# Optimization experiments

Hardware: AMD Instinct MI355X
Metric: run time of the kernel (lower is better)

## Reference

```python
import jax, jax.numpy as jnp
import numpy as np

KERNEL = 8


def setup_inputs() -> dict:
    key = jax.random.key(0)
    ks = jax.random.split(key, 9)
    N, Cin, L = 16, 128, 2048
    Cout = 256
    x = jax.random.normal(ks[0], (N, Cin, L), dtype=jnp.float32)
    conv_w = jax.random.normal(ks[1], (Cout, Cin, KERNEL), dtype=jnp.float32) * (1.0 / np.sqrt(Cin * KERNEL))
    conv_b = jax.random.normal(ks[2], (Cout,), dtype=jnp.float32) * 0.01
    wq = jax.random.normal(ks[3], (Cout, Cout), dtype=jnp.float32) * (1.0 / np.sqrt(Cout))
    bq = jax.random.normal(ks[4], (Cout,), dtype=jnp.float32) * 0.01
    wk = jax.random.normal(ks[5], (Cout, Cout), dtype=jnp.float32) * (1.0 / np.sqrt(Cout))
    bk = jax.random.normal(ks[6], (Cout,), dtype=jnp.float32) * 0.01
    wv = jax.random.normal(ks[7], (Cout, Cout), dtype=jnp.float32) * (1.0 / np.sqrt(Cout))
    bv = jax.random.normal(ks[8], (Cout,), dtype=jnp.float32) * 0.01
    return {"x": x, "conv_w": conv_w, "conv_b": conv_b,
            "wq": wq, "bq": bq, "wk": wk, "bk": bk, "wv": wv, "bv": bv}


def reference(x, conv_w, conv_b, wq, bq, wk, bk, wv, bv):
    # Conv1d, valid padding: [N, Cin, L] -> [N, Cout, S], S = L - KERNEL + 1
    h = jax.lax.conv_general_dilated(
        x, conv_w, window_strides=(1,), padding='VALID',
        dimension_numbers=('NCH', 'OIH', 'NCH'))
    h = jax.nn.relu(h + conv_b[None, :, None])
    N, C, S = h.shape
    h = jnp.transpose(h, (0, 2, 1))  # [N, S, C]
    # Linear layers (torch convention: y = x @ W^T + b)
    q = jnp.einsum('nsc,dc->nsd', h, wq) + bq
    k = jnp.einsum('nsc,dc->nsd', h, wk) + bk
    v = jnp.einsum('nsc,dc->nsd', h, wv) + bv
    # sigmoid (non-normalized) attention over full SxS scores
    scores = jnp.einsum('nsd,ntd->nst', q, k) / jnp.sqrt(jnp.asarray(C, h.dtype))
    attn = jax.nn.sigmoid(scores)  # [N, S, S]
    out = jnp.einsum('nst,ntd->nsd', attn, v)
    return jnp.transpose(out, (0, 2, 1))  # [N, C, S]
```

## Files before the change

### kernel.cpp

```cpp
#include <hip/hip_runtime.h>

typedef short short8 __attribute__((ext_vector_type(8)));
typedef float f32x4 __attribute__((ext_vector_type(4)));
typedef float f32x16 __attribute__((ext_vector_type(16)));
typedef unsigned short u16x4 __attribute__((ext_vector_type(4)));

constexpr int NB = 16, CIN = 128, LIN = 2048, CO = 256;
constexpr int SL = 2041;
constexpr int MT = NB * SL;
constexpr int MP = 32768;
constexpr int XTS = 136;

constexpr size_t XT_OFF = 0;
constexpr size_t XT_SZ  = (size_t)NB*LIN*XTS*2 + 65536;
constexpr size_t CW_OFF = XT_OFF + XT_SZ;
constexpr size_t CW_SZ  = (size_t)CO*CIN*8*2;
constexpr size_t WQ_OFF = CW_OFF + CW_SZ;
constexpr size_t WB_SZ  = (size_t)CO*CO*2;
constexpr size_t WK_OFF = WQ_OFF + WB_SZ;
constexpr size_t WV_OFF = WK_OFF + WB_SZ;
constexpr size_t H_OFF  = WV_OFF + WB_SZ;
constexpr size_t HB_SZ  = (size_t)MP*CO*2;
constexpr size_t Q_OFF  = H_OFF + HB_SZ;
constexpr size_t K_OFF  = Q_OFF + HB_SZ;
constexpr size_t VT_OFF = K_OFF + HB_SZ;

__device__ inline unsigned short f2bf(float f) {
  union { float f; unsigned int u; } v; v.f = f;
  unsigned int r = v.u + 0x7fffu + ((v.u >> 16) & 1u);
  return (unsigned short)(r >> 16);
}

__device__ inline void sync_lds() {
  __asm__ volatile("" ::: "memory");
  __builtin_amdgcn_s_waitcnt(0xc07f);
  __builtin_amdgcn_s_barrier();
  __asm__ volatile("" ::: "memory");
}
__device__ inline void barrier_only() {
  __asm__ volatile("" ::: "memory");
  __builtin_amdgcn_s_barrier();
  __asm__ volatile("" ::: "memory");
}

#if defined(__has_builtin)
#if __has_builtin(__builtin_amdgcn_global_load_lds)
#define HAVE_GLDS 1
#endif
#endif

__device__ inline void gld16(const unsigned short* g, void* l) {
#ifdef HAVE_GLDS
  __builtin_amdgcn_global_load_lds(
      (const __attribute__((address_space(1))) void*)g,
      (__attribute__((address_space(3))) void*)l, 16, 0, 0);
#else
  *(short8*)l = *(const short8*)g;
#endif
}

__global__ void xpose_kernel(const float* __restrict__ x, unsigned short* __restrict__ xt) {
  __shared__ float tile[32][33];
  const int tx = threadIdx.x, ty = threadIdx.y;
  const int s0 = blockIdx.x * 32, c0 = blockIdx.y * 32, n = blockIdx.z;
  #pragma unroll
  for (int r = 0; r < 4; ++r)
    tile[ty * 4 + r][tx] = x[((size_t)(n * CIN + c0 + ty * 4 + r)) * LIN + s0 + tx];
  __syncthreads();
  #pragma unroll
  for (int r = 0; r < 4; ++r)
    xt[((size_t)(n * LIN + s0 + ty * 4 + r)) * XTS + c0 + tx] = f2bf(tile[tx][ty * 4 + r]);
}

__global__ void wconv_kernel(const float* __restrict__ w, unsigned short* __restrict__ o) {
  int idx = blockIdx.x * 256 + threadIdx.x;
  int co = idx >> 10, r = idx & 1023, kp = r >> 7, ci = r & 127;
  o[idx] = f2bf(w[co * 1024 + ci * 8 + kp]);
}

__global__ void wqkv_kernel(const float* __restrict__ a, const float* __restrict__ b,
                            const float* __restrict__ c, unsigned short* __restrict__ oa,
                            unsigned short* __restrict__ ob, unsigned short* __restrict__ oc) {
  int z = blockIdx.x >> 6, lb = blockIdx.x & 63;
  const float* src = (z == 0) ? a : (z == 1) ? b : c;
  unsigned short* dst = (z == 0) ? oa : (z == 1) ? ob : oc;
  int i = (lb * 256 + threadIdx.x) * 4;
  float4 v = *(const float4*)(src + i);
  u16x4 r;
  r.x = f2bf(v.x); r.y = f2bf(v.y); r.z = f2bf(v.z); r.w = f2bf(v.w);
  *(u16x4*)(dst + i) = r;
}

__global__ __launch_bounds__(256) void conv_gemm(
    const unsigned short* __restrict__ xt,
    const unsigned short* __restrict__ wb,
    const float* __restrict__ bias,
    unsigned short* __restrict__ h)
{
  __shared__ unsigned short sX[18432];
  __shared__ unsigned short sB[2][4096];
  const int tid = threadIdx.x;
  const int w = tid >> 6, lane = tid & 63, quad = lane >> 4, l16 = lane & 15;
  const int n  = blockIdx.y;
  const int s0 = blockIdx.x * 128;
  const int d0 = blockIdx.z * 128;

  {
    const unsigned short* xbase = xt + ((size_t)n * LIN + s0) * XTS;
    #pragma unroll
    for (int i = 0; i < 9; ++i) {
      int u = i * 256 + tid;
      gld16(xbase + u * 8, ((char*)sX) + u * 16);
    }
  }

  const int brow0 = tid >> 2, bkgs = tid & 3;
  short8 breg[2];
  #pragma unroll
  for (int i2 = 0; i2 < 2; ++i2) {
    int row = i2 * 64 + brow0;
    int kg = bkgs ^ ((row >> 1) & 3);
    breg[i2] = *(const short8*)(wb + (size_t)(d0 + row) * 1024 + kg * 8);
  }
  #pragma unroll
  for (int i2 = 0; i2 < 2; ++i2)
    *(short8*)(&sB[0][(i2 * 256 + tid) * 8]) = breg[i2];
  __syncthreads();

  f32x4 acc[2][8];
  #pragma unroll
  for (int i = 0; i < 2; ++i)
    #pragma unroll
    for (int j = 0; j < 8; ++j) acc[i][j] = (f32x4){0.f, 0.f, 0.f, 0.f};

  for (int kc = 0; kc < 32; ++kc) {
    const int kcn = (kc < 31) ? kc + 1 : kc;
    const int kpn = kcn >> 2, ci0n = (kcn & 3) * 32;
    #pragma unroll
    for (int i2 = 0; i2 < 2; ++i2) {
      int row = i2 * 64 + brow0;
      int kg = bkgs ^ ((row >> 1) & 3);
      breg[i2] = *(const short8*)(wb + (size_t)(d0 + row) * 1024 + kpn * 128 + ci0n + kg * 8);
    }

    const int kp = kc >> 2, ci0 = (kc & 3) * 32;
    const unsigned short* sBc = sB[kc & 1];
    short8 bfr[8];
    #pragma unroll
    for (int j = 0; j < 8; ++j) {
      int r = j * 16 + l16;
      bfr[j] = *(const short8*)(sBc + r * 32 + (quad ^ ((r >> 1) & 3)) * 8);
    }
    #pragma unroll
    for (int i = 0; i < 2; ++i) {
      int srow = w * 32 + i * 16 + l16;
      short8 afr = *(const short8*)(sX + (srow + kp) * XTS + ci0 + quad * 8);
      #pragma unroll
      for (int j = 0; j < 8; ++j)
        acc[i][j] = __builtin_amdgcn_mfma_f32_16x16x32_bf16(afr, bfr[j], acc[i][j], 0, 0, 0);
    }

    #pragma unroll
    for (int i2 = 0; i2 < 2; ++i2)
      *(short8*)(&sB[(kc + 1) & 1][(i2 * 256 + tid) * 8]) = breg[i2];
    sync_lds();
  }

  #pragma unroll
  for (int i = 0; i < 2; ++i)
    #pragma unroll
    for (int j = 0; j < 8; ++j) {
      int col = d0 + j * 16 + l16;
      float bv = bias[col];
      #pragma unroll
      for (int jj = 0; jj < 4; ++jj) {
        int s = s0 + w * 32 + i * 16 + quad * 4 + jj;
        if (s < SL) {
          float val = fmaxf(acc[i][j][jj] + bv, 0.f);
          h[(size_t)(n * SL + s) * CO + col] = f2bf(val);
        }
      }
    }
}

__global__ __launch_bounds__(256) void lin_gemm(
    const unsigned short* __restrict__ A,
    const unsigned short* __restrict__ Bq, const unsigned short* __restrict__ Bk,
    const unsigned short* __restrict__ Bv,
    const float* __restrict__ biq, const float* __restrict__ bik,
    const float* __restrict__ biv,
    unsigned short* __restrict__ qb, unsigned short* __restrict__ kb,
    unsigned short* __restrict__ vtb)
{
  __shared__ unsigned short sA[2][4096];
  __shared__ unsigned short sB[2][4096];
  const int tid = threadIdx.x;
  const int w = tid >> 6, lane = tid & 63, quad = lane >> 4, l16 = lane & 15;
  const int m0 = blockIdx.x * 128, d0 = blockIdx.y * 128, z = blockIdx.z;
  const unsigned short* B = (z == 0) ? Bq : (z == 1) ? Bk : Bv;
  const float* bias        = (z == 0) ? biq : (z == 1) ? bik : biv;

  const int brow0 = tid >> 2, bkgs = tid & 3;
  short8 areg[2], breg[2];
  #pragma unroll
  for (int i2 = 0; i2 < 2; ++i2) {
    int row = i2 * 64 + brow0;
    int kg = bkgs ^ ((row >> 1) & 3);
    areg[i2] = *(const short8*)(A + (size_t)(m0 + row) * CO + kg * 8);
    breg[i2] = *(const short8*)(B + (size_t)(d0 + row) * CO + kg * 8);
  }
  #pragma unroll
  for (int i2 = 0; i2 < 2; ++i2) {
    *(short8*)(&sA[0][(i2 * 256 + tid) * 8]) = areg[i2];
    *(short8*)(&sB[0][(i2 * 256 + tid) * 8]) = breg[i2];
  }
  sync_lds();

  f32x4 acc[2][8];
  #pragma unroll
  for (int i = 0; i < 2; ++i)
    #pragma unroll
    for (int j = 0; j < 8; ++j) acc[i][j] = (f32x4){0.f, 0.f, 0.f, 0.f};

  for (int kc = 0; kc < 8; ++kc) {
    const int kcn = (kc < 7) ? kc + 1 : kc;
    #pragma unroll
    for (int i2 = 0; i2 < 2; ++i2) {
      int row = i2 * 64 + brow0;
      int kg = bkgs ^ ((row >> 1) & 3);
      areg[i2] = *(const short8*)(A + (size_t)(m0 + row) * CO + kcn * 32 + kg * 8);
      breg[i2] = *(const short8*)(B + (size_t)(d0 + row) * CO + kcn * 32 + kg * 8);
    }

    const unsigned short* sAc = sA[kc & 1];
    const unsigned short* sBc = sB[kc & 1];
    short8 afr[2], bfr[8];
    #pragma unroll
    for (int i = 0; i < 2; ++i) {
      int r = w * 32 + i * 16 + l16;
      afr[i] = *(const short8*)(sAc + r * 32 + (quad ^ ((r >> 1) & 3)) * 8);
    }
    #pragma unroll
    for (int j = 0; j < 8; ++j) {
      int r = j * 16 + l16;
      bfr[j] = *(const short8*)(sBc + r * 32 + (quad ^ ((r >> 1) & 3)) * 8);
    }
    #pragma unroll
    for (int i = 0; i < 2; ++i)
      #pragma unroll
      for (int j = 0; j < 8; ++j)
        acc[i][j] = __builtin_amdgcn_mfma_f32_16x16x32_bf16(afr[i], bfr[j], acc[i][j], 0, 0, 0);

    #pragma unroll
    for (int i2 = 0; i2 < 2; ++i2) {
      *(short8*)(&sA[(kc + 1) & 1][(i2 * 256 + tid) * 8]) = areg[i2];
      *(short8*)(&sB[(kc + 1) & 1][(i2 * 256 + tid) * 8]) = breg[i2];
    }
    sync_lds();
  }

  #pragma unroll
  for (int i = 0; i < 2; ++i)
    #pragma unroll
    for (int j = 0; j < 8; ++j) {
      int col = d0 + j * 16 + l16;
      float bv = bias[col];
      #pragma unroll
      for (int jj = 0; jj < 4; ++jj) {
        int m = m0 + w * 32 + i * 16 + quad * 4 + jj;
        float val = acc[i][j][jj] + bv;
        if (z < 2) {
          ((z == 0) ? qb : kb)[(size_t)m * CO + col] = f2bf(val);
        } else if (m < MT) {
          int nn = m / SL, ss = m - nn * SL;
          vtb[(size_t)col * MP + nn * 2048 + ss] = f2bf(val);
        }
      }
    }
}

__global__ __launch_bounds__(512, 2) void attn_kernel(
    const unsigned short* __restrict__ qb,
    const unsigned short* __restrict__ kb,
    const unsigned short* __restrict__ vtb,
    float* __restrict__ out)
{
  __shared__ unsigned short sK[2][16384];
  __shared__ unsigned short sV[2][16384];
  __shared__ unsigned short sP[8192];
  const int tid = threadIdx.x;
  const int w = tid >> 6, lane = tid & 63;
  const int half = lane >> 5, l32 = lane & 31;
  const int bidx = blockIdx.x;
  const int n = (bidx & 7) + ((bidx >> 7) << 3);
  const int s0 = ((bidx >> 3) & 15) * 128;
  const int sr = w & 3, tr = w >> 2;

  const unsigned short* kbN = kb + (size_t)(n * SL) * CO;
  const unsigned short* vbN = vtb + (size_t)n * 2048;

#define STAGE_TILE(buf, tk)                                                      \
  {                                                                              \
    _Pragma("unroll")                                                            \
    for (int i = 0; i < 4; ++i) {                                                \
      int u = i * 512 + tid;                                                     \
      int t = u >> 5, sl = u & 31;                                               \
      gld16(kbN + (size_t)((tk) + t) * CO + ((sl ^ (t & 31)) << 3),              \
            ((char*)sK[buf]) + u * 16);                                          \
    }                                                                            \
    _Pragma("unroll")                                                            \
    for (int i = 0; i < 4; ++i) {                                                \
      int u = i * 512 + tid;                                                     \
      int d = u >> 3, sl = u & 7;                                                \
      gld16(vbN + (size_t)d * MP + (tk) + ((sl ^ (d & 7)) << 3),                 \
            ((char*)sV[buf]) + u * 16);                                          \
    }                                                                            \
  }

  STAGE_TILE(0, 0)

  short8 qf[16];
  {
    const unsigned short* qp = qb + (size_t)(n * SL + s0 + sr * 32 + l32) * CO + half * 8;
    #pragma unroll
    for (int kk = 0; kk < 16; ++kk) qf[kk] = *(const short8*)(qp + kk * 16);
  }

  __builtin_amdgcn_s_waitcnt(0x0F70);
  barrier_only();

  f32x16 o[4];
  #pragma unroll
  for (int di = 0; di < 4; ++di)
    #pragma unroll
    for (int r = 0; r < 16; ++r) o[di][r] = 0.f;

  for (int it = 0; it < 32; ++it) {
    const int cur = it & 1;
    if (it < 31) {
      STAGE_TILE(cur ^ 1, (it + 1) * 64)
      __builtin_amdgcn_s_waitcnt(0x0F78);
    } else {
      __builtin_amdgcn_s_waitcnt(0x0F70);
    }
    barrier_only();

    const unsigned short* sKc = sK[cur];
    const int tl = tr * 32 + l32;
    f32x16 sacc;
    #pragma unroll
    for (int r = 0; r < 16; ++r) sacc[r] = 0.f;
    #pragma unroll
    for (int kk = 0; kk < 16; ++kk) {
      short8 kf = *(const short8*)(sKc + tl * 256 + (((kk * 2 + half) ^ (tl & 31)) << 3));
      sacc = __builtin_amdgcn_mfma_f32_32x32x16_bf16(kf, qf[kk], sacc, 0, 0, 0);
    }

    const int t0 = it * 64;
    #pragma unroll
    for (int q2 = 0; q2 < 4; ++q2) {
      u16x4 pk;
      #pragma unroll
      for (int e = 0; e < 4; ++e) {
        int tg = t0 + tr * 32 + 8 * q2 + 4 * half + e;
        float p = __builtin_amdgcn_rcpf(1.f + __expf(-sacc[q2 * 4 + e] * 0.0625f));
        pk[e] = (tg < SL) ? f2bf(p) : (unsigned short)0;
      }
      *(u16x4*)(sP + ((tr * 4 + q2) * 128 + sr * 32 + l32) * 8 + 4 * half) = pk;
    }
    sync_lds();

    const unsigned short* sVc = sV[cur];
    #pragma unroll
    for (int kt = 0; kt < 4; ++kt) {
      int g = kt * 2 + half;
      short8 pa = *(const short8*)(sP + ((g << 7) + sr * 32 + l32) * 8);
      #pragma unroll
      for (int di = 0; di < 4; ++di) {
        int d = tr * 128 + di * 32 + l32;
        short8 vf = *(const short8*)(sVc + d * 64 + ((g ^ (d & 7)) << 3));
        o[di] = __builtin_amdgcn_mfma_f32_32x32x16_bf16(vf, pa, o[di], 0, 0, 0);
      }
    }
    sync_lds();
  }

  const int s = s0 + sr * 32 + l32;
  if (s < SL) {
    float* op = out + (size_t)n * CO * SL + s;
    #pragma unroll
    for (int di = 0; di < 4; ++di)
      #pragma unroll
      for (int r = 0; r < 16; ++r) {
        int d = tr * 128 + di * 32 + (r & 3) + 8 * (r >> 2) + 4 * half;
        __builtin_nontemporal_store(o[di][r], op + (size_t)d * SL);
      }
  }
#undef STAGE_TILE
}

extern "C" void kernel_launch(void* const* d_in, const int* in_sizes, int n_in,
                              void* d_out, int out_size, void* d_ws, size_t ws_size,
                              hipStream_t stream) {
  const float* x      = (const float*)d_in[0];
  const float* conv_w = (const float*)d_in[1];
  const float* conv_b = (const float*)d_in[2];
  const float* wq     = (const float*)d_in[3];
  const float* bq     = (const float*)d_in[4];
  const float* wk     = (const float*)d_in[5];
  const float* bk     = (const float*)d_in[6];
  const float* wv     = (const float*)d_in[7];
  const float* bv     = (const float*)d_in[8];

  char* ws = (char*)d_ws;
  unsigned short* xt  = (unsigned short*)(ws + XT_OFF);
  unsigned short* cw  = (unsigned short*)(ws + CW_OFF);
  unsigned short* wqb = (unsigned short*)(ws + WQ_OFF);
  unsigned short* wkb = (unsigned short*)(ws + WK_OFF);
  unsigned short* wvb = (unsigned short*)(ws + WV_OFF);
  unsigned short* hb  = (unsigned short*)(ws + H_OFF);
  unsigned short* qb  = (unsigned short*)(ws + Q_OFF);
  unsigned short* kb  = (unsigned short*)(ws + K_OFF);
  unsigned short* vtb = (unsigned short*)(ws + VT_OFF);

  hipLaunchKernelGGL(xpose_kernel, dim3(64, 4, 16), dim3(32, 8), 0, stream, x, xt);
  hipLaunchKernelGGL(wconv_kernel, dim3(1024), dim3(256), 0, stream, conv_w, cw);
  hipLaunchKernelGGL(wqkv_kernel,  dim3(192), dim3(256), 0, stream,
                     wq, wk, wv, wqb, wkb, wvb);
  hipLaunchKernelGGL(conv_gemm, dim3(16, 16, 2), dim3(256), 0, stream, xt, cw, conv_b, hb);
  hipLaunchKernelGGL(lin_gemm,  dim3(256, 2, 3), dim3(256), 0, stream,
                     hb, wqb, wkb, wvb, bq, bk, bv, qb, kb, vtb);
  hipLaunchKernelGGL(attn_kernel, dim3(256), dim3(512), 0, stream,
                     qb, kb, vtb, (float*)d_out);
}
```

Measured before the change: 250.8 us.

## Keep sigmoid probabilities in registers and split PV over key halves

The 1/sqrt(C) scale is folded into the Q projection epilogue. The attention loop now converts sigmoid scores to bf16 in registers with packed convert and permlane32 swaps, so the LDS round-trip through sP is gone. Each warp group now accumulates all 256 output dims over its own half of the key tile instead of half the dims over all keys. The two partial outputs are reduced through LDS at the end. The prefetch wait moves to after the PV MFMAs and s_setprio is added around the MFMA blocks. This doubles the output accumulator registers (8 f32x16) and adds a final cross-warp reduction, which may raise register pressure under launch_bounds(512,2).

```diff
diff --git a/kernel.cpp b/kernel.cpp
--- a/kernel.cpp
+++ b/kernel.cpp
@@ -57,6 +57,15 @@
 #else
   *(short8*)l = *(const short8*)g;
 #endif
+}
+
+__device__ inline unsigned int cvt_pk_bf16(float a, float b) {
+  unsigned int r;
+  asm("v_cvt_pk_bf16_f32 %0, %1, %2" : "=v"(r) : "v"(a), "v"(b));
+  return r;
+}
+__device__ inline void swap32(unsigned int& a, unsigned int& b) {
+  asm("v_permlane32_swap_b32 %0, %1" : "+v"(a), "+v"(b));
 }
 
 __global__ void xpose_kernel(const float* __restrict__ x, unsigned short* __restrict__ xt) {
@@ -269,8 +278,10 @@
       for (int jj = 0; jj < 4; ++jj) {
         int m = m0 + w * 32 + i * 16 + quad * 4 + jj;
         float val = acc[i][j][jj] + bv;
-        if (z < 2) {
-          ((z == 0) ? qb : kb)[(size_t)m * CO + col] = f2bf(val);
+        if (z == 0) {
+          qb[(size_t)m * CO + col] = f2bf(val * 0.0625f);
+        } else if (z == 1) {
+          kb[(size_t)m * CO + col] = f2bf(val);
         } else if (m < MT) {
           int nn = m / SL, ss = m - nn * SL;
           vtb[(size_t)col * MP + nn * 2048 + ss] = f2bf(val);
@@ -287,7 +298,6 @@
 {
   __shared__ unsigned short sK[2][16384];
   __shared__ unsigned short sV[2][16384];
-  __shared__ unsigned short sP[8192];
   const int tid = threadIdx.x;
   const int w = tid >> 6, lane = tid & 63;
   const int half = lane >> 5, l32 = lane & 31;
@@ -329,72 +339,109 @@
   __builtin_amdgcn_s_waitcnt(0x0F70);
   barrier_only();
 
-  f32x16 o[4];
-  #pragma unroll
-  for (int di = 0; di < 4; ++di)
+  f32x16 o[8];
+  #pragma unroll
+  for (int di = 0; di < 8; ++di)
     #pragma unroll
     for (int r = 0; r < 16; ++r) o[di][r] = 0.f;
 
   for (int it = 0; it < 32; ++it) {
     const int cur = it & 1;
-    if (it < 31) {
-      STAGE_TILE(cur ^ 1, (it + 1) * 64)
-      __builtin_amdgcn_s_waitcnt(0x0F78);
-    } else {
-      __builtin_amdgcn_s_waitcnt(0x0F70);
-    }
-    barrier_only();
+    if (it < 31) STAGE_TILE(cur ^ 1, (it + 1) * 64)
 
     const unsigned short* sKc = sK[cur];
     const int tl = tr * 32 + l32;
     f32x16 sacc;
     #pragma unroll
     for (int r = 0; r < 16; ++r) sacc[r] = 0.f;
+    __builtin_amdgcn_s_setprio(1);
     #pragma unroll
     for (int kk = 0; kk < 16; ++kk) {
       short8 kf = *(const short8*)(sKc + tl * 256 + (((kk * 2 + half) ^ (tl & 31)) << 3));
       sacc = __builtin_amdgcn_mfma_f32_32x32x16_bf16(kf, qf[kk], sacc, 0, 0, 0);
     }
-
-    const int t0 = it * 64;
-    #pragma unroll
-    for (int q2 = 0; q2 < 4; ++q2) {
-      u16x4 pk;
-      #pragma unroll
-      for (int e = 0; e < 4; ++e) {
-        int tg = t0 + tr * 32 + 8 * q2 + 4 * half + e;
-        float p = __builtin_amdgcn_rcpf(1.f + __expf(-sacc[q2 * 4 + e] * 0.0625f));
-        pk[e] = (tg < SL) ? f2bf(p) : (unsigned short)0;
+    __builtin_amdgcn_s_setprio(0);
+
+    float p[16];
+    #pragma unroll
+    for (int r = 0; r < 16; ++r)
+      p[r] = __builtin_amdgcn_rcpf(1.f + __expf(-sacc[r]));
+    if (it == 31 && tr == 1) {
+      #pragma unroll
+      for (int r = 0; r < 16; ++r) {
+        int tloc = (r & 3) + 8 * (r >> 2) + 4 * half;
+        if (tloc >= 25) p[r] = 0.f;
       }
-      *(u16x4*)(sP + ((tr * 4 + q2) * 128 + sr * 32 + l32) * 8 + 4 * half) = pk;
-    }
+    }
+
+    short8 pa[2];
+    #pragma unroll
+    for (int kx = 0; kx < 2; ++kx) {
+      unsigned int x0 = cvt_pk_bf16(p[kx * 8 + 0], p[kx * 8 + 1]);
+      unsigned int x1 = cvt_pk_bf16(p[kx * 8 + 2], p[kx * 8 + 3]);
+      unsigned int y0 = cvt_pk_bf16(p[kx * 8 + 4], p[kx * 8 + 5]);
+      unsigned int y1 = cvt_pk_bf16(p[kx * 8 + 6], p[kx * 8 + 7]);
+      swap32(x0, y0);
+      swap32(x1, y1);
+      union { unsigned int u[4]; short8 s; } pu;
+      pu.u[0] = x0; pu.u[1] = x1; pu.u[2] = y0; pu.u[3] = y1;
+      pa[kx] = pu.s;
+    }
+
+    const unsigned short* sVc = sV[cur];
+    __builtin_amdgcn_s_setprio(1);
+    #pragma unroll
+    for (int kx = 0; kx < 2; ++kx) {
+      const int c8 = tr * 4 + kx * 2 + half;
+      #pragma unroll
+      for (int di = 0; di < 8; ++di) {
+        int d = di * 32 + l32;
+        short8 vf = *(const short8*)(sVc + d * 64 + ((c8 ^ (d & 7)) << 3));
+        o[di] = __builtin_amdgcn_mfma_f32_32x32x16_bf16(vf, pa[kx], o[di], 0, 0, 0);
+      }
+    }
+    __builtin_amdgcn_s_setprio(0);
+
+    if (it < 31) __builtin_amdgcn_s_waitcnt(0x0F70);
     sync_lds();
-
-    const unsigned short* sVc = sV[cur];
-    #pragma unroll
-    for (int kt = 0; kt < 4; ++kt) {
-      int g = kt * 2 + half;
-      short8 pa = *(const short8*)(sP + ((g << 7) + sr * 32 + l32) * 8);
-      #pragma unroll
-      for (int di = 0; di < 4; ++di) {
-        int d = tr * 128 + di * 32 + l32;
-        short8 vf = *(const short8*)(sVc + d * 64 + ((g ^ (d & 7)) << 3));
-        o[di] = __builtin_amdgcn_mfma_f32_32x32x16_bf16(vf, pa, o[di], 0, 0, 0);
+  }
+
+  {
+    unsigned short* myreg = (w < 4) ? (&sK[0][0] + (size_t)w * 8192)
+                                    : (&sV[0][0] + (size_t)(w - 4) * 8192);
+    const int sb = (tr ^ 1) * 4;
+    #pragma unroll
+    for (int di = 0; di < 4; ++di)
+      #pragma unroll
+      for (int q = 0; q < 4; ++q) {
+        f32x4 v;
+        #pragma unroll
+        for (int j = 0; j < 4; ++j) v[j] = o[sb + di][q * 4 + j];
+        *(f32x4*)((char*)myreg + (di * 4 + q) * 1024 + lane * 16) = v;
       }
-    }
-    sync_lds();
-  }
-
-  const int s = s0 + sr * 32 + l32;
-  if (s < SL) {
-    float* op = out + (size_t)n * CO * SL + s;
-    #pragma unroll
-    for (int di = 0; di < 4; ++di)
-      #pragma unroll
-      for (int r = 0; r < 16; ++r) {
-        int d = tr * 128 + di * 32 + (r & 3) + 8 * (r >> 2) + 4 * half;
-        __builtin_nontemporal_store(o[di][r], op + (size_t)d * SL);
-      }
+  }
+  sync_lds();
+  {
+    const int pw = w ^ 4;
+    const unsigned short* preg = (pw < 4) ? (&sK[0][0] + (size_t)pw * 8192)
+                                          : (&sV[0][0] + (size_t)(pw - 4) * 8192);
+    const int kb_ = tr * 4;
+    const int s = s0 + sr * 32 + l32;
+    if (s < SL) {
+      float* op = out + (size_t)n * CO * SL + s;
+      #pragma unroll
+      for (int di = 0; di < 4; ++di)
+        #pragma unroll
+        for (int q = 0; q < 4; ++q) {
+          f32x4 v = *(const f32x4*)((const char*)preg + (di * 4 + q) * 1024 + lane * 16);
+          #pragma unroll
+          for (int j = 0; j < 4; ++j) {
+            int r = q * 4 + j;
+            int d = (kb_ + di) * 32 + (r & 3) + 8 * (r >> 2) + 4 * half;
+            __builtin_nontemporal_store(o[kb_ + di][r] + v[j], op + (size_t)d * SL);
+          }
+        }
+    }
   }
 #undef STAGE_TILE
 }
```

Measured after the change: 263.5 us. 5.1% more time.
